# Kernel tuning notes

Measured on AMD Instinct MI355X. Metric: run time of the kernel, lower is better.

The kernel has to match this reference:

```python
import jax, jax.numpy as jnp
import numpy as np

B, T, D, H, O = 1024, 512, 64, 64, 32


def setup_inputs() -> dict:
    key = jax.random.key(0)
    ks = jax.random.split(key, 12)
    s = 1.0 / np.sqrt(H)  # torch LSTM/Linear default init scale
    u = lambda k, shape: jax.random.uniform(k, shape, jnp.float32, -s, s)
    return {
        "x": jax.random.normal(ks[0], (B, T, D), jnp.float32),
        # layer 0 (PyTorch gate order: i, f, g, o stacked along first dim)
        "w_ih0": u(ks[1], (4 * H, D)),
        "w_hh0": u(ks[2], (4 * H, H)),
        "b_ih0": u(ks[3], (4 * H,)),
        "b_hh0": u(ks[4], (4 * H,)),
        # layer 1
        "w_ih1": u(ks[5], (4 * H, H)),
        "w_hh1": u(ks[6], (4 * H, H)),
        "b_ih1": u(ks[7], (4 * H,)),
        "b_hh1": u(ks[8], (4 * H,)),
        # final linear head
        "fc_w": u(ks[9], (O, H)),
        "fc_b": u(ks[10], (O,)),
    }


def lstm_layer(x, w_ih, w_hh, b_ih, b_hh):
    """Single batch-first LSTM layer, PyTorch gate order (i, f, g, o)."""
    Bb = x.shape[0]
    Hh = w_hh.shape[1]
    # precompute input contribution for all timesteps: (B, T, 4H)
    pre = jnp.einsum('btd,gd->btg', x, w_ih) + b_ih + b_hh

    def step(carry, p_t):  # p_t: (B, 4H)
        h, c = carry
        gates = p_t + h @ w_hh.T
        i, f, g, o = jnp.split(gates, 4, axis=-1)
        c = jax.nn.sigmoid(f) * c + jax.nn.sigmoid(i) * jnp.tanh(g)
        h = jax.nn.sigmoid(o) * jnp.tanh(c)
        return (h, c), h

    h0 = jnp.zeros((Bb, Hh), x.dtype)
    (_, _), hs = jax.lax.scan(step, (h0, h0), jnp.swapaxes(pre, 0, 1))
    return jnp.swapaxes(hs, 0, 1)  # (B, T, H)


def reference(x, w_ih0, w_hh0, b_ih0, b_hh0, w_ih1, w_hh1, b_ih1, b_hh1, fc_w, fc_b):
    h1 = lstm_layer(x, w_ih0, w_hh0, b_ih0, b_hh0)
    h2 = lstm_layer(h1, w_ih1, w_hh1, b_ih1, b_hh1)
    last = h2[:, -1, :]  # (B, H)
    return jax.nn.softplus(last @ fc_w.T + fc_b)  # (B, O)
```

## Files before the change

### kernel.cpp

```cpp
#include <hip/hip_runtime.h>
#include <hip/hip_bf16.h>
#include <math.h>

#define BB 1024
#define TT 512
#define OO 32
#define MM 16
#define NBLK (BB/MM)

typedef __attribute__((ext_vector_type(8))) short short8;
typedef __attribute__((ext_vector_type(4))) float f32x4;

#define MFMA __builtin_amdgcn_mfma_f32_16x16x32_bf16
#define LOG2E 1.4426950408889634f
#define K2    2.8853900817779268f

#define BAR() asm volatile("s_waitcnt lgkmcnt(0)\n\ts_barrier" ::: "memory")

__device__ __forceinline__ float exp2f_(float x) {
#if __has_builtin(__builtin_amdgcn_exp2f)
    return __builtin_amdgcn_exp2f(x);
#else
    float r; asm("v_exp_f32 %0, %1" : "=v"(r) : "v"(x)); return r;
#endif
}

__device__ __forceinline__ ushort f2bf(float f) {
    union { float f; unsigned u; } v; v.f = f;
    unsigned r = v.u + 0x7FFF + ((v.u >> 16) & 1);
    return (ushort)(r >> 16);
}
__device__ __forceinline__ float bf2f(ushort u) {
    union { unsigned u; float f; } v; v.u = ((unsigned)u) << 16; return v.f;
}
__device__ __forceinline__ unsigned pkbf(float a, float b) {
    union { float f; unsigned u; } x, y; x.f = a; y.f = b;
    return __builtin_amdgcn_perm(y.u + 0x8000u, x.u + 0x8000u, 0x07060302u);
}
__device__ __forceinline__ short8 pack8(const float4& a, const float4& b) {
    union { unsigned u[4]; short8 s; } r;
    r.u[0] = pkbf(a.x, a.y); r.u[1] = pkbf(a.z, a.w);
    r.u[2] = pkbf(b.x, b.y); r.u[3] = pkbf(b.z, b.w);
    return r.s;
}

__global__ __launch_bounds__(512)
void lstm_fused8(const float* __restrict__ x,
                 const float* __restrict__ w_ih0,
                 const float* __restrict__ w_hh0,
                 const float* __restrict__ b_ih0,
                 const float* __restrict__ b_hh0,
                 const float* __restrict__ w_ih1,
                 const float* __restrict__ w_hh1,
                 const float* __restrict__ b_ih1,
                 const float* __restrict__ b_hh1,
                 const float* __restrict__ fc_w,
                 const float* __restrict__ fc_b,
                 float* __restrict__ out)
{
    __shared__ ushort h0s[2][MM][72];
    __shared__ ushort h1s[2][MM][72];

    const int tid  = threadIdx.x;
    const int wv   = tid >> 6;
    const bool gB  = (wv >= 4);
    const int u    = wv & 3;
    const int ln   = tid & 63;
    const int l15  = ln & 15;
    const int quad = ln >> 4;
    const int b0   = blockIdx.x * MM;
    const int hq   = 16 * u + l15;

    const float* wih = gB ? w_ih1 : w_ih0;
    const float* whh = gB ? w_hh1 : w_hh0;
    const float* bih = gB ? b_ih1 : b_ih0;
    const float* bhh = gB ? b_hh1 : b_hh0;

    short8 bfrag[4][4];
    float  biasv[4];
#pragma unroll
    for (int g = 0; g < 4; ++g) {
        const float sc = (g == 2) ? K2 : -LOG2E;
        const int col = 64 * g + 16 * u + l15;
        biasv[g] = (bih[col] + bhh[col]) * sc;
#pragma unroll
        for (int kt = 0; kt < 4; ++kt) {
            const int kb = kt * 32 + quad * 8;
            const float* src = (kb < 64) ? (wih + col * 64 + kb)
                                         : (whh + col * 64 + (kb - 64));
            const float4 v0 = *(const float4*)src;
            const float4 v1 = *(const float4*)(src + 4);
            short8 b;
            b[0] = (short)f2bf(v0.x * sc); b[1] = (short)f2bf(v0.y * sc);
            b[2] = (short)f2bf(v0.z * sc); b[3] = (short)f2bf(v0.w * sc);
            b[4] = (short)f2bf(v1.x * sc); b[5] = (short)f2bf(v1.y * sc);
            b[6] = (short)f2bf(v1.z * sc); b[7] = (short)f2bf(v1.w * sc);
            bfrag[g][kt] = b;
        }
    }

    const size_t xoff = ((size_t)(b0 + l15) * TT) * 64 + quad * 8;
    float4 xfA0, xfA1, xfA2, xfA3, xfB0, xfB1, xfB2, xfB3;

#define ISSUE(t_, S)                                                          \
    if ((t_) < TT) {                                                          \
        const float* p = x + xoff + (size_t)(t_) * 64;                        \
        xf##S##0 = *(const float4*)p;        xf##S##1 = *(const float4*)(p + 4);  \
        xf##S##2 = *(const float4*)(p + 32); xf##S##3 = *(const float4*)(p + 36); \
    }

    for (int i = tid; i < 2 * MM * 72; i += 512) {
        ((ushort*)h0s)[i] = 0;
        ((ushort*)h1s)[i] = 0;
    }
    if (!gB) { ISSUE(0, A); ISSUE(1, B); }

    float c0 = 0.f, c1 = 0.f, c2 = 0.f, c3 = 0.f;
    BAR();

#define CELL(ACC, CV, HROWS, R)                                               \
    {                                                                         \
        const float yi = ACC[0][R], yf = ACC[1][R];                           \
        const float yg = ACC[2][R], yo = ACC[3][R];                           \
        const float Ef = exp2f_(yf);                                          \
        const float Ei = exp2f_(yi);                                          \
        const float Eg = exp2f_(fminf(yg, 80.f));                             \
        const float sf = __builtin_amdgcn_rcpf(1.f + Ef);                     \
        const float rd = __builtin_amdgcn_rcpf((1.f + Ei) * (1.f + Eg));      \
        CV = sf * CV + (Eg - 1.f) * rd;                                       \
        const float Ec = exp2f_(fminf(CV * K2, 80.f));                        \
        const float Eo = exp2f_(yo);                                          \
        const float r2 = __builtin_amdgcn_rcpf((1.f + Eo) * (1.f + Ec));      \
        union { float f; unsigned uu; } hv; hv.f = (Ec - 1.f) * r2;           \
        HROWS[quad * 4 + R][hq] = (ushort)((hv.uu + 0x8000u) >> 16);          \
    }

#define STEP(t_, CUR, NXT, S, DOA, DOB)                                       \
    {                                                                         \
        if (!gB) {                                                            \
            if (DOA) {                                                        \
                const short8 a2 = *(const short8*)&h0s[CUR][l15][quad * 8];   \
                const short8 a3 = *(const short8*)&h0s[CUR][l15][32 + quad * 8]; \
                const short8 a0 = pack8(xf##S##0, xf##S##1);                  \
                const short8 a1 = pack8(xf##S##2, xf##S##3);                  \
                ISSUE((t_) + 2, S);                                           \
                f32x4 acc[4];                                                 \
                _Pragma("unroll")                                             \
                for (int g = 0; g < 4; ++g) {                                 \
                    f32x4 a = {biasv[g], biasv[g], biasv[g], biasv[g]};       \
                    a = MFMA(a0, bfrag[g][0], a, 0, 0, 0);                    \
                    a = MFMA(a1, bfrag[g][1], a, 0, 0, 0);                    \
                    a = MFMA(a2, bfrag[g][2], a, 0, 0, 0);                    \
                    a = MFMA(a3, bfrag[g][3], a, 0, 0, 0);                    \
                    acc[g] = a;                                               \
                }                                                             \
                CELL(acc, c0, h0s[NXT], 0); CELL(acc, c1, h0s[NXT], 1);       \
                CELL(acc, c2, h0s[NXT], 2); CELL(acc, c3, h0s[NXT], 3);       \
            }                                                                 \
        } else {                                                              \
            if (DOB) {                                                        \
                const short8 a0 = *(const short8*)&h0s[CUR][l15][quad * 8];   \
                const short8 a1 = *(const short8*)&h0s[CUR][l15][32 + quad * 8]; \
                const short8 a2 = *(const short8*)&h1s[CUR][l15][quad * 8];   \
                const short8 a3 = *(const short8*)&h1s[CUR][l15][32 + quad * 8]; \
                f32x4 acc[4];                                                 \
                _Pragma("unroll")                                             \
                for (int g = 0; g < 4; ++g) {                                 \
                    f32x4 a = {biasv[g], biasv[g], biasv[g], biasv[g]};       \
                    a = MFMA(a0, bfrag[g][0], a, 0, 0, 0);                    \
                    a = MFMA(a1, bfrag[g][1], a, 0, 0, 0);                    \
                    a = MFMA(a2, bfrag[g][2], a, 0, 0, 0);                    \
                    a = MFMA(a3, bfrag[g][3], a, 0, 0, 0);                    \
                    acc[g] = a;                                               \
                }                                                             \
                CELL(acc, c0, h1s[NXT], 0); CELL(acc, c1, h1s[NXT], 1);       \
                CELL(acc, c2, h1s[NXT], 2); CELL(acc, c3, h1s[NXT], 3);       \
            }                                                                 \
        }                                                                     \
        BAR();                                                                \
    }

    STEP(0, 0, 1, A, 1, 0)
    for (int tb = 1; tb + 2 < TT; tb += 2) {
        STEP(tb,     1, 0, B, 1, 1)
        STEP(tb + 1, 0, 1, A, 1, 1)
    }
    STEP(TT - 1, 1, 0, B, 1, 1)
    STEP(TT, 0, 1, A, 0, 1)
#undef STEP
#undef CELL
#undef ISSUE

    {
        const int row = tid >> 5, o = tid & 31;
        float a = fc_b[o];
#pragma unroll
        for (int j = 0; j < 64; ++j)
            a = fmaf(fc_w[o * 64 + j], bf2f(h1s[1][row][j]), a);
        out[(size_t)(b0 + row) * OO + o] =
            fmaxf(a, 0.0f) + log1pf(__expf(-fabsf(a)));
    }
}

extern "C" void kernel_launch(void* const* d_in, const int* in_sizes, int n_in,
                              void* d_out, int out_size, void* d_ws, size_t ws_size,
                              hipStream_t stream) {
    const float* x     = (const float*)d_in[0];
    const float* w_ih0 = (const float*)d_in[1];
    const float* w_hh0 = (const float*)d_in[2];
    const float* b_ih0 = (const float*)d_in[3];
    const float* b_hh0 = (const float*)d_in[4];
    const float* w_ih1 = (const float*)d_in[5];
    const float* w_hh1 = (const float*)d_in[6];
    const float* b_ih1 = (const float*)d_in[7];
    const float* b_hh1 = (const float*)d_in[8];
    const float* fc_w  = (const float*)d_in[9];
    const float* fc_b  = (const float*)d_in[10];
    float* out = (float*)d_out;

    lstm_fused8<<<dim3(NBLK), dim3(512), 0, stream>>>(
        x, w_ih0, w_hh0, b_ih0, b_hh0,
        w_ih1, w_hh1, b_ih1, b_hh1, fc_w, fc_b, out);
}
```

Baseline: 586.9 us.

## Shrink batch tile to 4 rows, precompute x projection off critical path

Cuts rows per block from 16 to 4, so the grid grows from 64 to 256 blocks and more CUs share the serial recurrence. MFMA tiles stay 16 wide with padded rows. Gate results are staged through shared memory so each lane runs a single cell update instead of four. The layer-0 input projection for the next step is computed after the current cell update, which takes it off the h-dependent chain. In exchange, most of each MFMA is wasted on padding and every step adds shared-memory round trips.

```diff
diff --git a/kernel.cpp b/kernel.cpp
--- a/kernel.cpp
+++ b/kernel.cpp
@@ -5,7 +5,7 @@
 #define BB 1024
 #define TT 512
 #define OO 32
-#define MM 16
+#define MM 4
 #define NBLK (BB/MM)
 
 typedef __attribute__((ext_vector_type(8))) short short8;
@@ -45,21 +45,22 @@
 }
 
 __global__ __launch_bounds__(512)
-void lstm_fused8(const float* __restrict__ x,
-                 const float* __restrict__ w_ih0,
-                 const float* __restrict__ w_hh0,
-                 const float* __restrict__ b_ih0,
-                 const float* __restrict__ b_hh0,
-                 const float* __restrict__ w_ih1,
-                 const float* __restrict__ w_hh1,
-                 const float* __restrict__ b_ih1,
-                 const float* __restrict__ b_hh1,
-                 const float* __restrict__ fc_w,
-                 const float* __restrict__ fc_b,
-                 float* __restrict__ out)
+void lstm_f256(const float* __restrict__ x,
+               const float* __restrict__ w_ih0,
+               const float* __restrict__ w_hh0,
+               const float* __restrict__ b_ih0,
+               const float* __restrict__ b_hh0,
+               const float* __restrict__ w_ih1,
+               const float* __restrict__ w_hh1,
+               const float* __restrict__ b_ih1,
+               const float* __restrict__ b_hh1,
+               const float* __restrict__ fc_w,
+               const float* __restrict__ fc_b,
+               float* __restrict__ out)
 {
-    __shared__ ushort h0s[2][MM][72];
-    __shared__ ushort h1s[2][MM][72];
+    __shared__ ushort h0s[2][16][72];
+    __shared__ ushort h1s[2][16][72];
+    __shared__ float  gsh[8][4][16][4];
 
     const int tid  = threadIdx.x;
     const int wv   = tid >> 6;
@@ -77,12 +78,13 @@
     const float* bhh = gB ? b_hh1 : b_hh0;
 
     short8 bfrag[4][4];
-    float  biasv[4];
+    f32x4  bias4[4];
 #pragma unroll
     for (int g = 0; g < 4; ++g) {
         const float sc = (g == 2) ? K2 : -LOG2E;
         const int col = 64 * g + 16 * u + l15;
-        biasv[g] = (bih[col] + bhh[col]) * sc;
+        const float bv = (bih[col] + bhh[col]) * sc;
+        bias4[g] = (f32x4){bv, bv, bv, bv};
 #pragma unroll
         for (int kt = 0; kt < 4; ++kt) {
             const int kb = kt * 32 + quad * 8;
@@ -99,8 +101,10 @@
         }
     }
 
-    const size_t xoff = ((size_t)(b0 + l15) * TT) * 64 + quad * 8;
+    const int xr = (l15 < MM) ? l15 : (MM - 1);
+    const size_t xoff = ((size_t)(b0 + xr) * TT) * 64 + quad * 8;
     float4 xfA0, xfA1, xfA2, xfA3, xfB0, xfB1, xfB2, xfB3;
+    f32x4 pre[4];
 
 #define ISSUE(t_, S)                                                          \
     if ((t_) < TT) {                                                          \
@@ -109,53 +113,69 @@
         xf##S##2 = *(const float4*)(p + 32); xf##S##3 = *(const float4*)(p + 36); \
     }
 
-    for (int i = tid; i < 2 * MM * 72; i += 512) {
+    for (int i = tid; i < 2 * 16 * 72; i += 512) {
         ((ushort*)h0s)[i] = 0;
         ((ushort*)h1s)[i] = 0;
     }
-    if (!gB) { ISSUE(0, A); ISSUE(1, B); }
-
-    float c0 = 0.f, c1 = 0.f, c2 = 0.f, c3 = 0.f;
+
+    float cc = 0.f;
+    if (!gB) {
+        ISSUE(0, A);
+        ISSUE(1, B);
+        const short8 xlo = pack8(xfA0, xfA1);
+        const short8 xhi = pack8(xfA2, xfA3);
+#pragma unroll
+        for (int g = 0; g < 4; ++g)
+            pre[g] = MFMA(xhi, bfrag[g][1],
+                          MFMA(xlo, bfrag[g][0], bias4[g], 0, 0, 0), 0, 0, 0);
+    }
     BAR();
 
-#define CELL(ACC, CV, HROWS, R)                                               \
+#define CELL1(HD, NXT)                                                        \
     {                                                                         \
-        const float yi = ACC[0][R], yf = ACC[1][R];                           \
-        const float yg = ACC[2][R], yo = ACC[3][R];                           \
+        const float yi = gsh[wv][0][l15][quad];                               \
+        const float yf = gsh[wv][1][l15][quad];                               \
+        const float yg = gsh[wv][2][l15][quad];                               \
+        const float yo = gsh[wv][3][l15][quad];                               \
         const float Ef = exp2f_(yf);                                          \
         const float Ei = exp2f_(yi);                                          \
         const float Eg = exp2f_(fminf(yg, 80.f));                             \
         const float sf = __builtin_amdgcn_rcpf(1.f + Ef);                     \
         const float rd = __builtin_amdgcn_rcpf((1.f + Ei) * (1.f + Eg));      \
-        CV = sf * CV + (Eg - 1.f) * rd;                                       \
-        const float Ec = exp2f_(fminf(CV * K2, 80.f));                        \
+        cc = sf * cc + (Eg - 1.f) * rd;                                       \
+        const float Ec = exp2f_(fminf(cc * K2, 80.f));                        \
         const float Eo = exp2f_(yo);                                          \
         const float r2 = __builtin_amdgcn_rcpf((1.f + Eo) * (1.f + Ec));      \
         union { float f; unsigned uu; } hv; hv.f = (Ec - 1.f) * r2;           \
-        HROWS[quad * 4 + R][hq] = (ushort)((hv.uu + 0x8000u) >> 16);          \
-    }
-
-#define STEP(t_, CUR, NXT, S, DOA, DOB)                                       \
+        HD[NXT][quad][hq] = (ushort)((hv.uu + 0x8000u) >> 16);                \
+    }
+
+#define STEP(t_, CUR, NXT, USE, LD, DOA, DOB)                                 \
     {                                                                         \
         if (!gB) {                                                            \
             if (DOA) {                                                        \
                 const short8 a2 = *(const short8*)&h0s[CUR][l15][quad * 8];   \
                 const short8 a3 = *(const short8*)&h0s[CUR][l15][32 + quad * 8]; \
-                const short8 a0 = pack8(xf##S##0, xf##S##1);                  \
-                const short8 a1 = pack8(xf##S##2, xf##S##3);                  \
-                ISSUE((t_) + 2, S);                                           \
                 f32x4 acc[4];                                                 \
                 _Pragma("unroll")                                             \
-                for (int g = 0; g < 4; ++g) {                                 \
-                    f32x4 a = {biasv[g], biasv[g], biasv[g], biasv[g]};       \
-                    a = MFMA(a0, bfrag[g][0], a, 0, 0, 0);                    \
-                    a = MFMA(a1, bfrag[g][1], a, 0, 0, 0);                    \
-                    a = MFMA(a2, bfrag[g][2], a, 0, 0, 0);                    \
-                    a = MFMA(a3, bfrag[g][3], a, 0, 0, 0);                    \
-                    acc[g] = a;                                               \
-                }                                                             \
-                CELL(acc, c0, h0s[NXT], 0); CELL(acc, c1, h0s[NXT], 1);       \
-                CELL(acc, c2, h0s[NXT], 2); CELL(acc, c3, h0s[NXT], 3);       \
+                for (int g = 0; g < 4; ++g)                                   \
+                    acc[g] = MFMA(a3, bfrag[g][3],                            \
+                                  MFMA(a2, bfrag[g][2], pre[g], 0,0,0), 0,0,0); \
+                if (quad == 0) {                                              \
+                    _Pragma("unroll")                                         \
+                    for (int g = 0; g < 4; ++g)                               \
+                        *(f32x4*)&gsh[wv][g][l15][0] = acc[g];                \
+                }                                                             \
+                ISSUE((t_) + 2, LD);                                          \
+                CELL1(h0s, NXT);                                              \
+                if ((t_) + 1 < TT) {                                          \
+                    const short8 xlo = pack8(xf##USE##0, xf##USE##1);         \
+                    const short8 xhi = pack8(xf##USE##2, xf##USE##3);         \
+                    _Pragma("unroll")                                         \
+                    for (int g = 0; g < 4; ++g)                               \
+                        pre[g] = MFMA(xhi, bfrag[g][1],                       \
+                                      MFMA(xlo, bfrag[g][0], bias4[g], 0,0,0), 0,0,0); \
+                }                                                             \
             }                                                                 \
         } else {                                                              \
             if (DOB) {                                                        \
@@ -166,32 +186,36 @@
                 f32x4 acc[4];                                                 \
                 _Pragma("unroll")                                             \
                 for (int g = 0; g < 4; ++g) {                                 \
-                    f32x4 a = {biasv[g], biasv[g], biasv[g], biasv[g]};       \
+                    f32x4 a = bias4[g];                                       \
                     a = MFMA(a0, bfrag[g][0], a, 0, 0, 0);                    \
                     a = MFMA(a1, bfrag[g][1], a, 0, 0, 0);                    \
                     a = MFMA(a2, bfrag[g][2], a, 0, 0, 0);                    \
                     a = MFMA(a3, bfrag[g][3], a, 0, 0, 0);                    \
                     acc[g] = a;                                               \
                 }                                                             \
-                CELL(acc, c0, h1s[NXT], 0); CELL(acc, c1, h1s[NXT], 1);       \
-                CELL(acc, c2, h1s[NXT], 2); CELL(acc, c3, h1s[NXT], 3);       \
+                if (quad == 0) {                                              \
+                    _Pragma("unroll")                                         \
+                    for (int g = 0; g < 4; ++g)                               \
+                        *(f32x4*)&gsh[wv][g][l15][0] = acc[g];                \
+                }                                                             \
+                CELL1(h1s, NXT);                                              \
             }                                                                 \
         }                                                                     \
         BAR();                                                                \
     }
 
-    STEP(0, 0, 1, A, 1, 0)
+    STEP(0, 0, 1, B, A, 1, 0)
     for (int tb = 1; tb + 2 < TT; tb += 2) {
-        STEP(tb,     1, 0, B, 1, 1)
-        STEP(tb + 1, 0, 1, A, 1, 1)
-    }
-    STEP(TT - 1, 1, 0, B, 1, 1)
-    STEP(TT, 0, 1, A, 0, 1)
+        STEP(tb,     1, 0, A, B, 1, 1)
+        STEP(tb + 1, 0, 1, B, A, 1, 1)
+    }
+    STEP(TT - 1, 1, 0, A, B, 1, 1)
+    STEP(TT, 0, 1, B, A, 0, 1)
 #undef STEP
-#undef CELL
+#undef CELL1
 #undef ISSUE
 
-    {
+    if (tid < MM * OO) {
         const int row = tid >> 5, o = tid & 31;
         float a = fc_b[o];
 #pragma unroll
@@ -218,7 +242,7 @@
     const float* fc_b  = (const float*)d_in[10];
     float* out = (float*)d_out;
 
-    lstm_fused8<<<dim3(NBLK), dim3(512), 0, stream>>>(
+    lstm_f256<<<dim3(NBLK), dim3(512), 0, stream>>>(
         x, w_ih0, w_hh0, b_ih0, b_hh0,
         w_ih1, w_hh1, b_ih1, b_hh1, fc_w, fc_b, out);
 }
```

After: 556.9 us. 1.05x faster.

## Shrink batch tile to two rows per block to occupy all CUs

Applied to the files above, without the earlier changes.

Reduces the batch rows per block from 16 to 2 and the block size from 512 to 256 threads, launching 512 blocks instead of 64 so the whole GPU is used. Each wave now covers 32 hidden units with two MFMA n-tiles, and each lane selects the single accumulator element for its own (row, unit) pair, keeping one cell state per lane. This spreads the serial recurrence across many more CUs at the cost of mostly wasted rows in each 16-row MFMA tile and more total weight loading.

```diff
diff --git a/kernel.cpp b/kernel.cpp
--- a/kernel.cpp
+++ b/kernel.cpp
@@ -5,7 +5,7 @@
 #define BB 1024
 #define TT 512
 #define OO 32
-#define MM 16
+#define MM 2
 #define NBLK (BB/MM)
 
 typedef __attribute__((ext_vector_type(8))) short short8;
@@ -44,62 +44,69 @@
     return r.s;
 }
 
-__global__ __launch_bounds__(512)
-void lstm_fused8(const float* __restrict__ x,
-                 const float* __restrict__ w_ih0,
-                 const float* __restrict__ w_hh0,
-                 const float* __restrict__ b_ih0,
-                 const float* __restrict__ b_hh0,
-                 const float* __restrict__ w_ih1,
-                 const float* __restrict__ w_hh1,
-                 const float* __restrict__ b_ih1,
-                 const float* __restrict__ b_hh1,
-                 const float* __restrict__ fc_w,
-                 const float* __restrict__ fc_b,
-                 float* __restrict__ out)
+__global__ __launch_bounds__(256, 2)
+void lstm_v7(const float* __restrict__ x,
+             const float* __restrict__ w_ih0,
+             const float* __restrict__ w_hh0,
+             const float* __restrict__ b_ih0,
+             const float* __restrict__ b_hh0,
+             const float* __restrict__ w_ih1,
+             const float* __restrict__ w_hh1,
+             const float* __restrict__ b_ih1,
+             const float* __restrict__ b_hh1,
+             const float* __restrict__ fc_w,
+             const float* __restrict__ fc_b,
+             float* __restrict__ out)
 {
     __shared__ ushort h0s[2][MM][72];
     __shared__ ushort h1s[2][MM][72];
 
     const int tid  = threadIdx.x;
     const int wv   = tid >> 6;
-    const bool gB  = (wv >= 4);
-    const int u    = wv & 3;
+    const bool gB  = (wv >= 2);
+    const int w    = wv & 1;
     const int ln   = tid & 63;
     const int l15  = ln & 15;
     const int quad = ln >> 4;
     const int b0   = blockIdx.x * MM;
-    const int hq   = 16 * u + l15;
+
+    const bool qb0 = (quad & 1) != 0;
+    const bool qb1 = (quad & 2) != 0;
+    const int  hrow = quad & 1;
+    const int  hu   = 32 * w + 16 * (quad >> 1) + l15;
 
     const float* wih = gB ? w_ih1 : w_ih0;
     const float* whh = gB ? w_hh1 : w_hh0;
     const float* bih = gB ? b_ih1 : b_ih0;
     const float* bhh = gB ? b_hh1 : b_hh0;
 
-    short8 bfrag[4][4];
-    float  biasv[4];
+    short8 bfrag[4][2][4];
+    float  bias_c[4];
 #pragma unroll
     for (int g = 0; g < 4; ++g) {
         const float sc = (g == 2) ? K2 : -LOG2E;
-        const int col = 64 * g + 16 * u + l15;
-        biasv[g] = (bih[col] + bhh[col]) * sc;
-#pragma unroll
-        for (int kt = 0; kt < 4; ++kt) {
-            const int kb = kt * 32 + quad * 8;
-            const float* src = (kb < 64) ? (wih + col * 64 + kb)
-                                         : (whh + col * 64 + (kb - 64));
-            const float4 v0 = *(const float4*)src;
-            const float4 v1 = *(const float4*)(src + 4);
-            short8 b;
-            b[0] = (short)f2bf(v0.x * sc); b[1] = (short)f2bf(v0.y * sc);
-            b[2] = (short)f2bf(v0.z * sc); b[3] = (short)f2bf(v0.w * sc);
-            b[4] = (short)f2bf(v1.x * sc); b[5] = (short)f2bf(v1.y * sc);
-            b[6] = (short)f2bf(v1.z * sc); b[7] = (short)f2bf(v1.w * sc);
-            bfrag[g][kt] = b;
+        bias_c[g] = (bih[64 * g + hu] + bhh[64 * g + hu]) * sc;
+#pragma unroll
+        for (int n = 0; n < 2; ++n) {
+            const int col = 64 * g + 32 * w + 16 * n + l15;
+#pragma unroll
+            for (int kt = 0; kt < 4; ++kt) {
+                const int kb = kt * 32 + quad * 8;
+                const float* src = (kb < 64) ? (wih + col * 64 + kb)
+                                             : (whh + col * 64 + (kb - 64));
+                const float4 v0 = *(const float4*)src;
+                const float4 v1 = *(const float4*)(src + 4);
+                short8 b;
+                b[0] = (short)f2bf(v0.x * sc); b[1] = (short)f2bf(v0.y * sc);
+                b[2] = (short)f2bf(v0.z * sc); b[3] = (short)f2bf(v0.w * sc);
+                b[4] = (short)f2bf(v1.x * sc); b[5] = (short)f2bf(v1.y * sc);
+                b[6] = (short)f2bf(v1.z * sc); b[7] = (short)f2bf(v1.w * sc);
+                bfrag[g][n][kt] = b;
+            }
         }
     }
 
-    const size_t xoff = ((size_t)(b0 + l15) * TT) * 64 + quad * 8;
+    const size_t xoff = ((size_t)(b0 + (l15 & 1)) * TT) * 64 + quad * 8;
     float4 xfA0, xfA1, xfA2, xfA3, xfB0, xfB1, xfB2, xfB3;
 
 #define ISSUE(t_, S)                                                          \
@@ -109,72 +116,76 @@
         xf##S##2 = *(const float4*)(p + 32); xf##S##3 = *(const float4*)(p + 36); \
     }
 
-    for (int i = tid; i < 2 * MM * 72; i += 512) {
+    for (int i = tid; i < 2 * MM * 72; i += 256) {
         ((ushort*)h0s)[i] = 0;
         ((ushort*)h1s)[i] = 0;
     }
     if (!gB) { ISSUE(0, A); ISSUE(1, B); }
 
-    float c0 = 0.f, c1 = 0.f, c2 = 0.f, c3 = 0.f;
+    const f32x4 z4 = {0.f, 0.f, 0.f, 0.f};
+    float cc = 0.f;
     BAR();
 
-#define CELL(ACC, CV, HROWS, R)                                               \
+#define YSEL(g) ((qb1 ? (qb0 ? acc[g][1][1] : acc[g][1][0])                   \
+                      : (qb0 ? acc[g][0][1] : acc[g][0][0])) + bias_c[g])
+
+#define CELL(HD, NXT)                                                         \
     {                                                                         \
-        const float yi = ACC[0][R], yf = ACC[1][R];                           \
-        const float yg = ACC[2][R], yo = ACC[3][R];                           \
+        const float yi = YSEL(0), yf = YSEL(1);                               \
+        const float yg = YSEL(2), yo = YSEL(3);                               \
         const float Ef = exp2f_(yf);                                          \
         const float Ei = exp2f_(yi);                                          \
         const float Eg = exp2f_(fminf(yg, 80.f));                             \
         const float sf = __builtin_amdgcn_rcpf(1.f + Ef);                     \
         const float rd = __builtin_amdgcn_rcpf((1.f + Ei) * (1.f + Eg));      \
-        CV = sf * CV + (Eg - 1.f) * rd;                                       \
-        const float Ec = exp2f_(fminf(CV * K2, 80.f));                        \
+        cc = sf * cc + (Eg - 1.f) * rd;                                       \
+        const float Ec = exp2f_(fminf(cc * K2, 80.f));                        \
         const float Eo = exp2f_(yo);                                          \
         const float r2 = __builtin_amdgcn_rcpf((1.f + Eo) * (1.f + Ec));      \
         union { float f; unsigned uu; } hv; hv.f = (Ec - 1.f) * r2;           \
-        HROWS[quad * 4 + R][hq] = (ushort)((hv.uu + 0x8000u) >> 16);          \
+        HD[NXT][hrow][hu] = (ushort)((hv.uu + 0x8000u) >> 16);                \
     }
 
 #define STEP(t_, CUR, NXT, S, DOA, DOB)                                       \
     {                                                                         \
         if (!gB) {                                                            \
             if (DOA) {                                                        \
-                const short8 a2 = *(const short8*)&h0s[CUR][l15][quad * 8];   \
-                const short8 a3 = *(const short8*)&h0s[CUR][l15][32 + quad * 8]; \
-                const short8 a0 = pack8(xf##S##0, xf##S##1);                  \
-                const short8 a1 = pack8(xf##S##2, xf##S##3);                  \
+                const short8 a2 = *(const short8*)&h0s[CUR][l15 & 1][quad * 8];      \
+                const short8 a3 = *(const short8*)&h0s[CUR][l15 & 1][32 + quad * 8]; \
+                const short8 xlo = pack8(xf##S##0, xf##S##1);                 \
+                const short8 xhi = pack8(xf##S##2, xf##S##3);                 \
                 ISSUE((t_) + 2, S);                                           \
-                f32x4 acc[4];                                                 \
+                f32x4 acc[4][2];                                              \
                 _Pragma("unroll")                                             \
                 for (int g = 0; g < 4; ++g) {                                 \
-                    f32x4 a = {biasv[g], biasv[g], biasv[g], biasv[g]};       \
-                    a = MFMA(a0, bfrag[g][0], a, 0, 0, 0);                    \
-                    a = MFMA(a1, bfrag[g][1], a, 0, 0, 0);                    \
-                    a = MFMA(a2, bfrag[g][2], a, 0, 0, 0);                    \
-                    a = MFMA(a3, bfrag[g][3], a, 0, 0, 0);                    \
-                    acc[g] = a;                                               \
+                    _Pragma("unroll")                                         \
+                    for (int n = 0; n < 2; ++n)                               \
+                        acc[g][n] =                                           \
+                          MFMA(a3, bfrag[g][n][3],                            \
+                          MFMA(a2, bfrag[g][n][2],                            \
+                          MFMA(xhi, bfrag[g][n][1],                           \
+                          MFMA(xlo, bfrag[g][n][0], z4, 0,0,0), 0,0,0), 0,0,0), 0,0,0); \
                 }                                                             \
-                CELL(acc, c0, h0s[NXT], 0); CELL(acc, c1, h0s[NXT], 1);       \
-                CELL(acc, c2, h0s[NXT], 2); CELL(acc, c3, h0s[NXT], 3);       \
+                CELL(h0s, NXT);                                               \
             }                                                                 \
         } else {                                                              \
             if (DOB) {                                                        \
-                const short8 a0 = *(const short8*)&h0s[CUR][l15][quad * 8];   \
-                const short8 a1 = *(const short8*)&h0s[CUR][l15][32 + quad * 8]; \
-                const short8 a2 = *(const short8*)&h1s[CUR][l15][quad * 8];   \
-                const short8 a3 = *(const short8*)&h1s[CUR][l15][32 + quad * 8]; \
-                f32x4 acc[4];                                                 \
+                const short8 a0 = *(const short8*)&h0s[CUR][l15 & 1][quad * 8];      \
+                const short8 a1 = *(const short8*)&h0s[CUR][l15 & 1][32 + quad * 8]; \
+                const short8 a2 = *(const short8*)&h1s[CUR][l15 & 1][quad * 8];      \
+                const short8 a3 = *(const short8*)&h1s[CUR][l15 & 1][32 + quad * 8]; \
+                f32x4 acc[4][2];                                              \
                 _Pragma("unroll")                                             \
                 for (int g = 0; g < 4; ++g) {                                 \
-                    f32x4 a = {biasv[g], biasv[g], biasv[g], biasv[g]};       \
-                    a = MFMA(a0, bfrag[g][0], a, 0, 0, 0);                    \
-                    a = MFMA(a1, bfrag[g][1], a, 0, 0, 0);                    \
-                    a = MFMA(a2, bfrag[g][2], a, 0, 0, 0);                    \
-                    a = MFMA(a3, bfrag[g][3], a, 0, 0, 0);                    \
-                    acc[g] = a;                                               \
+                    _Pragma("unroll")                                         \
+                    for (int n = 0; n < 2; ++n)                               \
+                        acc[g][n] =                                           \
+                          MFMA(a3, bfrag[g][n][3],                            \
+                          MFMA(a2, bfrag[g][n][2],                            \
+                          MFMA(a1, bfrag[g][n][1],                            \
+                          MFMA(a0, bfrag[g][n][0], z4, 0,0,0), 0,0,0), 0,0,0), 0,0,0); \
                 }                                                             \
-                CELL(acc, c0, h1s[NXT], 0); CELL(acc, c1, h1s[NXT], 1);       \
-                CELL(acc, c2, h1s[NXT], 2); CELL(acc, c3, h1s[NXT], 3);       \
+                CELL(h1s, NXT);                                               \
             }                                                                 \
         }                                                                     \
         BAR();                                                                \
@@ -189,9 +200,10 @@
     STEP(TT, 0, 1, A, 0, 1)
 #undef STEP
 #undef CELL
+#undef YSEL
 #undef ISSUE
 
-    {
+    if (tid < MM * OO) {
         const int row = tid >> 5, o = tid & 31;
         float a = fc_b[o];
 #pragma unroll
@@ -218,7 +230,7 @@
     const float* fc_b  = (const float*)d_in[10];
     float* out = (float*)d_out;
 
-    lstm_fused8<<<dim3(NBLK), dim3(512), 0, stream>>>(
+    lstm_v7<<<dim3(NBLK), dim3(256), 0, stream>>>(
         x, w_ih0, w_hh0, b_ih0, b_hh0,
         w_ih1, w_hh1, b_ih1, b_hh1, fc_w, fc_b, out);
 }
```

Result: faster. 569.9 us (-2.9%).
